# Kernel tuning notes

Measured on AMD Instinct MI355X. Metric: run time of the kernel, lower is better.

Reference implementation:

```python
import jax, jax.numpy as jnp
import numpy as np

N_NODES = 100000


def _add_self_loops(edge_index, n):
    loop = jnp.arange(n, dtype=edge_index.dtype)
    src = jnp.concatenate([edge_index[0], loop])
    dst = jnp.concatenate([edge_index[1], loop])
    return src, dst


def _gcn_conv(x, W, b, src, dst, n):
    # PyG GCNConv: add_self_loops + symmetric normalization + linear + scatter-add
    deg = jax.ops.segment_sum(jnp.ones_like(dst, dtype=x.dtype), dst, num_segments=n)
    dinv = jnp.where(deg > 0, jax.lax.rsqrt(deg), 0.0)
    h = x @ W  # [N, F_out]
    norm = dinv[src] * dinv[dst]            # [E]
    msg = h[src] * norm[:, None]            # gather + scale, [E, F_out]
    out = jax.ops.segment_sum(msg, dst, num_segments=n)
    return out + b


def setup_inputs() -> dict:
    key = jax.random.key(0)
    k1, k2, k3, k4 = jax.random.split(key, 4)
    d = 128
    E = 1600000
    x = jax.random.normal(k1, (N_NODES, d), dtype=jnp.float32)
    edge_index = jax.random.randint(k2, (2, E), 0, N_NODES, dtype=jnp.int64)
    # Glorot-ish scaling for the linear weights
    s = 1.0 / np.sqrt(d)
    W1 = jax.random.normal(k3, (d, d), dtype=jnp.float32) * s
    W2 = jax.random.normal(k4, (d, d), dtype=jnp.float32) * s
    b1 = jnp.zeros((d,), dtype=jnp.float32)
    b2 = jnp.zeros((d,), dtype=jnp.float32)
    return {"x": x, "edge_index": edge_index, "W1": W1, "b1": b1, "W2": W2, "b2": b2}


def reference(x, edge_index, W1, b1, W2, b2):
    n = x.shape[0]
    src, dst = _add_self_loops(edge_index, n)
    h = jax.nn.relu(_gcn_conv(x, W1, b1, src, dst, n))
    out = _gcn_conv(h, W2, b2, src, dst, n)
    # original does x.view(1600) (= N * out_channels for its 40x40 toy size);
    # generalized: flatten to [N * out_channels]
    return out.reshape(-1)
```

## Files before the change

### kernel.cpp

```cpp
#include <hip/hip_runtime.h>

static inline int idiv_up(int a, int b) { return (a + b - 1) / b; }

typedef __attribute__((ext_vector_type(8))) short bf16x8;
typedef __attribute__((ext_vector_type(4))) float f32x4;

#define NBSHIFT 9
#define BCAP    11264
#define EPB     4096

__device__ __forceinline__ float bf16u_to_f32(unsigned short u) {
    return __uint_as_float(((unsigned int)u) << 16);
}

__device__ __forceinline__ unsigned short f32_to_bf16u(float x) {
    unsigned int b = __float_as_uint(x);
    b += 0x7FFFu + ((b >> 16) & 1u);
    return (unsigned short)(b >> 16);
}

__global__ void k_binit(int* __restrict__ bucketCur) {
    if (threadIdx.x < 256) bucketCur[threadIdx.x] = threadIdx.x * BCAP;
}

__global__ __launch_bounds__(256) void k_bucketA(const int* __restrict__ src,
                                                 const int* __restrict__ dst, int E,
                                                 int* __restrict__ bucketCur,
                                                 int* __restrict__ tmp) {
    __shared__ int bh[256];
    __shared__ int bbase[256];
    const int tid = threadIdx.x;
    const int c0 = blockIdx.x * EPB;
    const int cend = min(c0 + EPB, E);
    bh[tid] = 0;
    __syncthreads();

    int sv[16], dv[16];
#pragma unroll
    for (int i = 0; i < 4; ++i) {
        const int p = c0 + i * 1024 + tid * 4;
        int4 s4 = make_int4(0, 0, 0, 0);
        int4 d4 = make_int4(-1, -1, -1, -1);
        if (p + 4 <= cend) {
            s4 = *(const int4*)(src + p);
            d4 = *(const int4*)(dst + p);
        } else if (p < cend) {
            s4.x = src[p]; d4.x = dst[p];
            if (p + 1 < cend) { s4.y = src[p + 1]; d4.y = dst[p + 1]; }
            if (p + 2 < cend) { s4.z = src[p + 2]; d4.z = dst[p + 2]; }
        }
        sv[i * 4 + 0] = s4.x; sv[i * 4 + 1] = s4.y; sv[i * 4 + 2] = s4.z; sv[i * 4 + 3] = s4.w;
        dv[i * 4 + 0] = d4.x; dv[i * 4 + 1] = d4.y; dv[i * 4 + 2] = d4.z; dv[i * 4 + 3] = d4.w;
    }
#pragma unroll
    for (int i = 0; i < 16; ++i)
        if (dv[i] >= 0) atomicAdd(&bh[dv[i] >> NBSHIFT], 1);
    __syncthreads();
    {
        const int c = bh[tid];
        bbase[tid] = c ? atomicAdd(&bucketCur[tid], c) : 0;
        bh[tid] = 0;
    }
    __syncthreads();
#pragma unroll
    for (int i = 0; i < 16; ++i) {
        if (dv[i] >= 0) {
            const int b = dv[i] >> NBSHIFT;
            const int loc = atomicAdd(&bh[b], 1);
            tmp[bbase[b] + loc] = ((dv[i] & ((1 << NBSHIFT) - 1)) << 17) | sv[i];
        }
    }
}

__global__ __launch_bounds__(512) void k_build(const int* __restrict__ tmp,
                                               const int* __restrict__ bucketCur,
                                               int2* __restrict__ rowcnt,
                                               float* __restrict__ dinv,
                                               int* __restrict__ csr, int N) {
    __shared__ int h[512];
    __shared__ int woff[9];
    const int b = blockIdx.x;
    const int tid = threadIdx.x;
    const int beg = b * BCAP;
    const int ecnt = bucketCur[b] - beg;
    const int node0 = b << NBSHIFT;

    h[tid] = 0;
    __syncthreads();
    for (int i = tid; i < ecnt; i += 512)
        atomicAdd(&h[tmp[beg + i] >> 17], 1);
    __syncthreads();

    const int v = h[tid];
    const int lane = tid & 63;
    const int w = tid >> 6;
    int incl = v;
#pragma unroll
    for (int off = 1; off < 64; off <<= 1) {
        const int y = __shfl_up(incl, off, 64);
        if (lane >= off) incl += y;
    }
    if (lane == 63) woff[w + 1] = incl;
    if (tid == 0) woff[0] = 0;
    __syncthreads();
    if (tid == 0) {
#pragma unroll
        for (int i = 1; i < 8; ++i) woff[i + 1] += woff[i];
    }
    __syncthreads();
    const int rowbase = beg + woff[w] + incl - v;
    const int node = node0 + tid;
    if (node < N) {
        rowcnt[node] = make_int2(rowbase, v);
        dinv[node]   = rsqrtf((float)v + 1.0f);
    }
    __syncthreads();
    h[tid] = rowbase;
    __syncthreads();
    for (int i = tid; i < ecnt; i += 512) {
        const int p = tmp[beg + i];
        const int pos = atomicAdd(&h[p >> 17], 1);
        csr[pos] = p & 0x1FFFF;
    }
}

template<bool ABF16>
__global__ __launch_bounds__(256) void k_gemm(const void* __restrict__ Av,
                                              const float* __restrict__ W,
                                              const float* __restrict__ dinv,
                                              unsigned short* __restrict__ C, int N) {
    __shared__ unsigned short Wt[128 * 128];
    const int tid = threadIdx.x;

    {
        const int col = tid >> 1;
        const int k0  = (tid & 1) * 64;
#pragma unroll
        for (int i = 0; i < 8; ++i) {
            bf16x8 pk;
#pragma unroll
            for (int j = 0; j < 8; ++j)
                pk[j] = (short)f32_to_bf16u(W[(size_t)(k0 + i * 8 + j) * 128 + col]);
            const int kus = k0 + i * 8;
            *(bf16x8*)&Wt[col * 128 + (kus ^ ((col & 7) << 3))] = pk;
        }
    }
    __syncthreads();

    const int wave = tid >> 6;
    const int lane = tid & 63;
    const int lrow = lane & 15;
    const int lgrp = lane >> 4;
    const int rbase = blockIdx.x * 128 + wave * 32;

    f32x4 acc[2][8];
#pragma unroll
    for (int r = 0; r < 2; ++r)
#pragma unroll
        for (int c = 0; c < 8; ++c) acc[r][c] = (f32x4){0.f, 0.f, 0.f, 0.f};

#pragma unroll
    for (int kk = 0; kk < 4; ++kk) {
        const int kbase = kk * 32 + lgrp * 8;
        bf16x8 afrag[2];
#pragma unroll
        for (int r = 0; r < 2; ++r) {
            const int row = rbase + r * 16 + lrow;
            bf16x8 a = (bf16x8){0, 0, 0, 0, 0, 0, 0, 0};
            if (row < N) {
                if constexpr (ABF16) {
                    a = *(const bf16x8*)((const unsigned short*)Av + (size_t)row * 128 + kbase);
                } else {
                    const float* p = (const float*)Av + (size_t)row * 128 + kbase;
                    const float4 f0 = *(const float4*)p;
                    const float4 f1 = *(const float4*)(p + 4);
                    a[0] = (short)f32_to_bf16u(f0.x); a[1] = (short)f32_to_bf16u(f0.y);
                    a[2] = (short)f32_to_bf16u(f0.z); a[3] = (short)f32_to_bf16u(f0.w);
                    a[4] = (short)f32_to_bf16u(f1.x); a[5] = (short)f32_to_bf16u(f1.y);
                    a[6] = (short)f32_to_bf16u(f1.z); a[7] = (short)f32_to_bf16u(f1.w);
                }
            }
            afrag[r] = a;
        }
#pragma unroll
        for (int c = 0; c < 8; ++c) {
            const int col = c * 16 + lrow;
            const bf16x8 bb = *(const bf16x8*)&Wt[col * 128 + (kbase ^ ((col & 7) << 3))];
            acc[0][c] = __builtin_amdgcn_mfma_f32_16x16x32_bf16(afrag[0], bb, acc[0][c], 0, 0, 0);
            acc[1][c] = __builtin_amdgcn_mfma_f32_16x16x32_bf16(afrag[1], bb, acc[1][c], 0, 0, 0);
        }
    }

#pragma unroll
    for (int r = 0; r < 2; ++r) {
#pragma unroll
        for (int reg = 0; reg < 4; ++reg) {
            const int orow = rbase + r * 16 + lgrp * 4 + reg;
            if (orow < N) {
                const float dv = dinv[orow];
                unsigned short* crow = C + (size_t)orow * 128 + lrow;
#pragma unroll
                for (int c = 0; c < 8; ++c)
                    crow[c * 16] = f32_to_bf16u(acc[r][c][reg] * dv);
            }
        }
    }
}

template<int OUT_BF16_RELU>
__global__ __launch_bounds__(256) void k_pull(const int2* __restrict__ rowcnt,
                                              const int* __restrict__ csr,
                                              const unsigned short* __restrict__ t,
                                              const float* __restrict__ dinv,
                                              const float* __restrict__ bias,
                                              void* __restrict__ outv, int N) {
    const int nid = blockIdx.x * 4 + (threadIdx.x >> 6);
    if (nid >= N) return;
    const int lane2 = (threadIdx.x & 63) * 2;
    const int2 rc = rowcnt[nid];
    const int beg = rc.x;
    const int end = rc.x + rc.y;

    const float dd = dinv[nid];
    const ushort2 us = *(const ushort2*)(t + (size_t)nid * 128 + lane2);
    const float2 bvec = *(const float2*)(bias + lane2);

    float acc0 = 0.f, acc1 = 0.f;
    int j = beg;

    for (; j + 16 <= end; j += 16) {
        int s[16];
#pragma unroll
        for (int q = 0; q < 16; ++q) s[q] = csr[j + q];
        ushort2 u[16];
#pragma unroll
        for (int q = 0; q < 16; ++q)
            u[q] = *(const ushort2*)(t + (size_t)s[q] * 128 + lane2);
#pragma unroll
        for (int q = 0; q < 16; ++q) {
            acc0 += bf16u_to_f32(u[q].x);
            acc1 += bf16u_to_f32(u[q].y);
        }
    }
    if (j + 8 <= end) {
        int s[8];
#pragma unroll
        for (int q = 0; q < 8; ++q) s[q] = csr[j + q];
        ushort2 u[8];
#pragma unroll
        for (int q = 0; q < 8; ++q)
            u[q] = *(const ushort2*)(t + (size_t)s[q] * 128 + lane2);
#pragma unroll
        for (int q = 0; q < 8; ++q) {
            acc0 += bf16u_to_f32(u[q].x);
            acc1 += bf16u_to_f32(u[q].y);
        }
        j += 8;
    }
    if (j + 4 <= end) {
        int s[4];
#pragma unroll
        for (int q = 0; q < 4; ++q) s[q] = csr[j + q];
        ushort2 u[4];
#pragma unroll
        for (int q = 0; q < 4; ++q)
            u[q] = *(const ushort2*)(t + (size_t)s[q] * 128 + lane2);
#pragma unroll
        for (int q = 0; q < 4; ++q) {
            acc0 += bf16u_to_f32(u[q].x);
            acc1 += bf16u_to_f32(u[q].y);
        }
        j += 4;
    }
    for (; j + 2 <= end; j += 2) {
        const int s0 = csr[j];
        const int s1 = csr[j + 1];
        const ushort2 u0 = *(const ushort2*)(t + (size_t)s0 * 128 + lane2);
        const ushort2 u1 = *(const ushort2*)(t + (size_t)s1 * 128 + lane2);
        acc0 += bf16u_to_f32(u0.x); acc1 += bf16u_to_f32(u0.y);
        acc0 += bf16u_to_f32(u1.x); acc1 += bf16u_to_f32(u1.y);
    }
    if (j < end) {
        const ushort2 u = *(const ushort2*)(t + (size_t)csr[j] * 128 + lane2);
        acc0 += bf16u_to_f32(u.x); acc1 += bf16u_to_f32(u.y);
    }

    acc0 = (acc0 + bf16u_to_f32(us.x)) * dd + bvec.x;
    acc1 = (acc1 + bf16u_to_f32(us.y)) * dd + bvec.y;
    if (OUT_BF16_RELU) {
        acc0 = fmaxf(acc0, 0.f); acc1 = fmaxf(acc1, 0.f);
        ushort2 o; o.x = f32_to_bf16u(acc0); o.y = f32_to_bf16u(acc1);
        *(ushort2*)((unsigned short*)outv + (size_t)nid * 128 + lane2) = o;
    } else {
        *(float2*)((float*)outv + (size_t)nid * 128 + lane2) = make_float2(acc0, acc1);
    }
}

extern "C" void kernel_launch(void* const* d_in, const int* in_sizes, int n_in,
                              void* d_out, int out_size, void* d_ws, size_t ws_size,
                              hipStream_t stream) {
    const float* x   = (const float*)d_in[0];
    const int*   ei  = (const int*)d_in[1];
    const float* W1  = (const float*)d_in[2];
    const float* b1  = (const float*)d_in[3];
    const float* W2  = (const float*)d_in[4];
    const float* b2  = (const float*)d_in[5];
    float*       out = (float*)d_out;

    const int N = in_sizes[0] / 128;
    const int E = in_sizes[1] / 2;
    const int* esrc = ei;
    const int* edst = ei + E;
    const size_t NF = (size_t)N * 128;
    const int nbk = idiv_up(N, 1 << NBSHIFT);
    const int ebl = idiv_up(E, EPB);

    char* ws = (char*)d_ws;
    size_t o = 0;
    int*   bucketCur = (int*)(ws + o);   o += 256 * 4;              o = (o + 255) & ~(size_t)255;
    int2*  rowcnt    = (int2*)(ws + o);  o += (size_t)N * 8;        o = (o + 255) & ~(size_t)255;
    float* dinv      = (float*)(ws + o); o += (size_t)N * 4;        o = (o + 255) & ~(size_t)255;
    unsigned short* t = (unsigned short*)(ws + o); o += NF * 2;     o = (o + 255) & ~(size_t)255;
    unsigned short* h = (unsigned short*)(ws + o); o += NF * 2;     o = (o + 255) & ~(size_t)255;
    int*   tmp       = (int*)(ws + o);   o += (size_t)(nbk + 1) * BCAP * 4; o = (o + 255) & ~(size_t)255;
    int*   csr       = (int*)(ws + o);   o += (size_t)(nbk + 1) * BCAP * 4;

    k_binit  <<<1, 256, 0, stream>>>(bucketCur);
    k_bucketA<<<ebl, 256, 0, stream>>>(esrc, edst, E, bucketCur, tmp);
    k_build  <<<nbk, 512, 0, stream>>>(tmp, bucketCur, rowcnt, dinv, csr, N);

    const int gblocks = idiv_up(N, 128);
    const int pblocks = idiv_up(N, 4);

    k_gemm<false><<<gblocks, 256, 0, stream>>>(x, W1, dinv, t, N);
    k_pull<1>    <<<pblocks, 256, 0, stream>>>(rowcnt, csr, t, dinv, b1, h, N);

    k_gemm<true> <<<gblocks, 256, 0, stream>>>(h, W2, dinv, t, N);
    k_pull<0>    <<<pblocks, 256, 0, stream>>>(rowcnt, csr, t, dinv, b2, out, N);
}
```

Before: 209.9 us.

## Slice pull aggregation by feature columns across blocks for cache locality

The gather-sum kernel is restructured so each block handles one of eight 16-feature slices (32 bytes per row) for eight nodes. Within a wave, groups of eight lanes process different edges in parallel and are combined with cross-lane shuffles. Adjacent blocks share a node chunk and each reads a different column slice. The aim is to shrink the per-row footprint touched per pass so the feature table's working set stays L2-resident, and to spread edges across lanes. The cost is many more blocks, a reduction step, 32-byte sector gathers, and eight separate reads of the CSR indices.

Result: slower. 545.7 us (+159.9%).

```diff
diff --git a/kernel.cpp b/kernel.cpp
--- a/kernel.cpp
+++ b/kernel.cpp
@@ -214,85 +214,57 @@
                                               const float* __restrict__ dinv,
                                               const float* __restrict__ bias,
                                               void* __restrict__ outv, int N) {
-    const int nid = blockIdx.x * 4 + (threadIdx.x >> 6);
-    if (nid >= N) return;
-    const int lane2 = (threadIdx.x & 63) * 2;
-    const int2 rc = rowcnt[nid];
-    const int beg = rc.x;
-    const int end = rc.x + rc.y;
-
-    const float dd = dinv[nid];
-    const ushort2 us = *(const ushort2*)(t + (size_t)nid * 128 + lane2);
-    const float2 bvec = *(const float2*)(bias + lane2);
-
-    float acc0 = 0.f, acc1 = 0.f;
-    int j = beg;
-
-    for (; j + 16 <= end; j += 16) {
-        int s[16];
-#pragma unroll
-        for (int q = 0; q < 16; ++q) s[q] = csr[j + q];
-        ushort2 u[16];
-#pragma unroll
-        for (int q = 0; q < 16; ++q)
-            u[q] = *(const ushort2*)(t + (size_t)s[q] * 128 + lane2);
-#pragma unroll
-        for (int q = 0; q < 16; ++q) {
-            acc0 += bf16u_to_f32(u[q].x);
-            acc1 += bf16u_to_f32(u[q].y);
-        }
-    }
-    if (j + 8 <= end) {
-        int s[8];
-#pragma unroll
-        for (int q = 0; q < 8; ++q) s[q] = csr[j + q];
-        ushort2 u[8];
-#pragma unroll
-        for (int q = 0; q < 8; ++q)
-            u[q] = *(const ushort2*)(t + (size_t)s[q] * 128 + lane2);
-#pragma unroll
-        for (int q = 0; q < 8; ++q) {
-            acc0 += bf16u_to_f32(u[q].x);
-            acc1 += bf16u_to_f32(u[q].y);
-        }
-        j += 8;
-    }
-    if (j + 4 <= end) {
-        int s[4];
-#pragma unroll
-        for (int q = 0; q < 4; ++q) s[q] = csr[j + q];
-        ushort2 u[4];
-#pragma unroll
-        for (int q = 0; q < 4; ++q)
-            u[q] = *(const ushort2*)(t + (size_t)s[q] * 128 + lane2);
-#pragma unroll
-        for (int q = 0; q < 4; ++q) {
-            acc0 += bf16u_to_f32(u[q].x);
-            acc1 += bf16u_to_f32(u[q].y);
-        }
-        j += 4;
-    }
-    for (; j + 2 <= end; j += 2) {
-        const int s0 = csr[j];
-        const int s1 = csr[j + 1];
-        const ushort2 u0 = *(const ushort2*)(t + (size_t)s0 * 128 + lane2);
-        const ushort2 u1 = *(const ushort2*)(t + (size_t)s1 * 128 + lane2);
-        acc0 += bf16u_to_f32(u0.x); acc1 += bf16u_to_f32(u0.y);
-        acc0 += bf16u_to_f32(u1.x); acc1 += bf16u_to_f32(u1.y);
-    }
-    if (j < end) {
-        const ushort2 u = *(const ushort2*)(t + (size_t)csr[j] * 128 + lane2);
-        acc0 += bf16u_to_f32(u.x); acc1 += bf16u_to_f32(u.y);
-    }
-
-    acc0 = (acc0 + bf16u_to_f32(us.x)) * dd + bvec.x;
-    acc1 = (acc1 + bf16u_to_f32(us.y)) * dd + bvec.y;
-    if (OUT_BF16_RELU) {
-        acc0 = fmaxf(acc0, 0.f); acc1 = fmaxf(acc1, 0.f);
-        ushort2 o; o.x = f32_to_bf16u(acc0); o.y = f32_to_bf16u(acc1);
-        *(ushort2*)((unsigned short*)outv + (size_t)nid * 128 + lane2) = o;
-    } else {
-        *(float2*)((float*)outv + (size_t)nid * 128 + lane2) = make_float2(acc0, acc1);
+    const int slice = blockIdx.x & 7;
+    const int chunk = blockIdx.x >> 3;
+    const int wave  = threadIdx.x >> 6;
+    const int lane  = threadIdx.x & 63;
+    const int g     = lane >> 3;
+    const int l     = lane & 7;
+    const int f0    = slice * 16;
+    const unsigned short* ts = t + f0 + l * 2;
+
+    const float2 bv = *(const float2*)(bias + f0 + l * 2);
+
+#pragma unroll
+    for (int sub = 0; sub < 2; ++sub) {
+        const int nid = chunk * 8 + wave * 2 + sub;
+        if (nid >= N) continue;
+        const int2 rc = rowcnt[nid];
+        const int end = rc.x + rc.y;
+        const float dd = dinv[nid];
+        const ushort2 us = *(const ushort2*)(ts + (size_t)nid * 128);
+
+        float a0 = 0.f, a1 = 0.f;
+        int j = rc.x + g;
+        for (; j + 8 < end; j += 16) {
+            const int s0 = csr[j];
+            const int s1 = csr[j + 8];
+            const ushort2 u0 = *(const ushort2*)(ts + (size_t)s0 * 128);
+            const ushort2 u1 = *(const ushort2*)(ts + (size_t)s1 * 128);
+            a0 += bf16u_to_f32(u0.x) + bf16u_to_f32(u1.x);
+            a1 += bf16u_to_f32(u0.y) + bf16u_to_f32(u1.y);
+        }
+        if (j < end) {
+            const ushort2 u = *(const ushort2*)(ts + (size_t)csr[j] * 128);
+            a0 += bf16u_to_f32(u.x);
+            a1 += bf16u_to_f32(u.y);
+        }
+#pragma unroll
+        for (int m = 8; m <= 32; m <<= 1) {
+            a0 += __shfl_xor(a0, m, 64);
+            a1 += __shfl_xor(a1, m, 64);
+        }
+        a0 = (a0 + bf16u_to_f32(us.x)) * dd + bv.x;
+        a1 = (a1 + bf16u_to_f32(us.y)) * dd + bv.y;
+        if (lane < 8) {
+            if (OUT_BF16_RELU) {
+                a0 = fmaxf(a0, 0.f); a1 = fmaxf(a1, 0.f);
+                ushort2 o; o.x = f32_to_bf16u(a0); o.y = f32_to_bf16u(a1);
+                *(ushort2*)((unsigned short*)outv + (size_t)nid * 128 + f0 + l * 2) = o;
+            } else {
+                *(float2*)((float*)outv + (size_t)nid * 128 + f0 + l * 2) = make_float2(a0, a1);
+            }
+        }
     }
 }
 
@@ -330,7 +302,7 @@
     k_build  <<<nbk, 512, 0, stream>>>(tmp, bucketCur, rowcnt, dinv, csr, N);
 
     const int gblocks = idiv_up(N, 128);
-    const int pblocks = idiv_up(N, 4);
+    const int pblocks = idiv_up(N, 8) * 8;
 
     k_gemm<false><<<gblocks, 256, 0, stream>>>(x, W1, dinv, t, N);
     k_pull<1>    <<<pblocks, 256, 0, stream>>>(rowcnt, csr, t, dinv, b1, h, N);
```
